# Kernel optimization log

Hardware: AMD Instinct MI355X
Metric: run time of the kernel (lower is better)

The kernel has to match this reference:

```python
import jax, jax.numpy as jnp
import numpy as np

B, T, H, L, V, S = 64, 256, 512, 64, 500, 3
TEMP_B = 1.0
EPS = 1e-17
NEG_INF = -1e9


def setup_inputs() -> dict:
    key = jax.random.key(0)
    ks = jax.random.split(key, 20)
    s = 0.02
    actions = jax.random.randint(ks[0], (B, T), 0, V)
    lengths = jax.random.randint(ks[1], (B,), 1, T + 1)
    u = jax.random.uniform(ks[2], (S - 1, B, T), minval=1e-6, maxval=1.0 - 1e-6)
    gumbel_b = -jnp.log(-jnp.log(u))                      # Gumbel(0,1) noise for boundary sampling
    eps_z = jax.random.normal(ks[3], (S, B, L))            # N(0,1) noise for gaussian latents
    embed = jax.random.normal(ks[4], (V, H)) * s
    Wx = jax.random.normal(ks[5], (H, 4 * H)) * s          # LSTM kernel (gate order i,f,g,o)
    Wh = jax.random.normal(ks[6], (H, 4 * H)) * s          # LSTM recurrent kernel
    b_lstm = jnp.zeros((4 * H,)).at[H:2 * H].set(1.0)      # unit forget bias (keras default)
    Wz1 = jax.random.normal(ks[7], (H, H)) * s
    bz1 = jnp.zeros((H,))
    Wz2 = jax.random.normal(ks[8], (H, 2 * L)) * s         # gaussian head -> [mu, log_var]
    bz2 = jnp.zeros((2 * L,))
    Wb1 = jax.random.normal(ks[9], (H, H)) * s
    bb1 = jnp.zeros((H,))
    Wb2 = jax.random.normal(ks[10], (H, 1)) * s
    bb2 = jnp.zeros((1,))
    Wd1 = jax.random.normal(ks[11], (L, H)) * s
    bd1 = jnp.zeros((H,))
    Wd2 = jax.random.normal(ks[12], (H, V)) * s
    bd2 = jnp.zeros((V,))
    return dict(actions=actions, lengths=lengths, gumbel_b=gumbel_b, eps_z=eps_z,
                embed=embed, Wx=Wx, Wh=Wh, b_lstm=b_lstm,
                Wz1=Wz1, bz1=bz1, Wz2=Wz2, bz2=bz2,
                Wb1=Wb1, bb1=bb1, Wb2=Wb2, bb2=bb2,
                Wd1=Wd1, bd1=bd1, Wd2=Wd2, bd2=bd2)


def _masked_encode(x, mask, Wx, Wh, b):
    """Masked LSTM: state is multiplied by mask[:, t] after every step."""
    def step(carry, inp):
        h, c = carry
        x_t, m_t = inp
        z = x_t @ Wx + h @ Wh + b
        i, f, g, o = jnp.split(z, 4, axis=-1)
        c_new = jax.nn.sigmoid(f) * c + jax.nn.sigmoid(i) * jnp.tanh(g)
        h_new = jax.nn.sigmoid(o) * jnp.tanh(c_new)
        m = m_t[:, None]
        return (m * h_new, m * c_new), h_new  # outputs are pre-mask h (as in source)
    h0 = jnp.zeros((x.shape[0], Wh.shape[0]), x.dtype)
    _, outs = jax.lax.scan(step, (h0, h0), (jnp.swapaxes(x, 0, 1), mask.T))
    return jnp.swapaxes(outs, 0, 1)  # [B,T,H]


def reference(actions, lengths, gumbel_b, eps_z, embed, Wx, Wh, b_lstm,
              Wz1, bz1, Wz2, bz2, Wb1, bb1, Wb2, bb2, Wd1, bd1, Wd2, bd2):
    emb = embed[actions]                       # [B,T,H]
    mask = jnp.ones((B, T), emb.dtype)
    encs, recs, masks = [], [], []
    logits_b_all, sample_b_all = [], []
    logits_z_all, sample_z_all = [], []
    for seg in range(S):
        enc = _masked_encode(emb, mask, Wx, Wh, b_lstm)
        encs.append(enc)
        if seg == S - 1:
            sample_b = jax.nn.one_hot(lengths - 1, T, dtype=emb.dtype)
        else:
            hid = jax.nn.relu(enc @ Wb1 + bb1)
            logits = (hid @ Wb2 + bb2)[..., 0]            # [B,T]
            logits = jnp.concatenate(
                [jnp.full((B, 1), NEG_INF, logits.dtype), logits[:, 1:]], axis=1)
            sample_b = jax.nn.softmax((logits + gumbel_b[seg]) / TEMP_B, axis=1)
            logits_b_all.append(logits)
        sample_b_all.append(sample_b)
        # latent readout (segment endpoint weighted sum)
        readout = jnp.sum(enc[:, :-1] * sample_b[:, 1:, None], axis=1)  # [B,H]
        hz = jax.nn.relu(readout @ Wz1 + bz1)
        logits_z = hz @ Wz2 + bz2                          # [B,2L]
        mu, log_var = jnp.split(logits_z, 2, axis=1)
        sample_z = mu + jnp.exp(0.5 * log_var) * eps_z[seg]
        logits_z_all.append(logits_z)
        sample_z_all.append(sample_z)
        # next-segment RNN mask: product of cumsums of all boundary samples so far
        if seg < S - 1:
            log_cums = [jnp.log(jnp.cumsum(bb, axis=1) + EPS) for bb in sample_b_all]
            mask = jnp.exp(sum(log_cums))
            masks.append(mask)
        # decode: single step from z, repeated over full sequence
        hd = jax.nn.relu(sample_z @ Wd1 + bd1)
        pred = hd @ Wd2 + bd2                              # [B,V]
        recs.append(jnp.broadcast_to(pred[:, None, :], (B, T, V)))
    return (jnp.stack(encs), jnp.stack(recs), jnp.stack(masks),
            jnp.stack(logits_b_all), jnp.stack(sample_b_all),
            jnp.stack(logits_z_all), jnp.stack(sample_z_all))
```

## Files before the change

### kernel.cpp

```cpp
#include <hip/hip_runtime.h>
#include <cstdint>
#include <cstddef>

typedef unsigned short ubf;
typedef unsigned int   u32;
typedef __attribute__((ext_vector_type(8))) short short8;
typedef __attribute__((ext_vector_type(4))) float f32x4;
typedef __attribute__((ext_vector_type(4))) float f4v;
typedef __attribute__((ext_vector_type(2))) float f2v;
typedef __attribute__((ext_vector_type(4))) unsigned short us4;

#define NEG_INF_F (-1000000000.0f)
#define FOURH 2048

#define ENC_SEG   8388608
#define REC_OFF   25165824
#define REC_SEG   8192000
#define MASK_OFF  49741824
#define LOGB_OFF  49774592
#define SAMB_OFF  49807360
#define LOGZ_OFF  49856512
#define SAMZ_OFF  49881088

#define SCR_P       0
#define SCR_HBUF    524288
#define SCR_FLAGS   557056
#define SCR_MASKF   558080
#define SCR_LOGCUM  574464
#define SCR_PART    590848
#define SCR_ENCB    1048576

__device__ __forceinline__ float bf2f(ubf u){
  union { u32 i; float f; } v; v.i = ((u32)u) << 16; return v.f;
}
__device__ __forceinline__ ubf f2bf(float f){
  union { float f; u32 i; } v; v.f = f;
  u32 x = v.i;
  u32 r = (x + 0x7FFFu + ((x >> 16) & 1u)) >> 16;
  return (ubf)r;
}
__device__ __forceinline__ float sigm(float x){
  return 1.0f / (1.0f + __expf(-x));
}
__device__ __forceinline__ float tanh_fast(float x){
  x = fminf(fmaxf(x, -20.0f), 20.0f);
  float e2 = __expf(2.0f * x);
  return (e2 - 1.0f) / (e2 + 1.0f);
}

__global__ void init_kernel(u32* flags){
  int tid = threadIdx.x;
  #pragma unroll
  for (int i = 0; i < 4; i++) flags[tid + i*256] = 0u;
}

__global__ __launch_bounds__(256, 2) void gemm_kernel(
    const void* __restrict__ Aptr, int a_f32,
    const float* __restrict__ Bf, const float* __restrict__ bias,
    ubf* __restrict__ C, const float* __restrict__ wb2, float* __restrict__ part,
    int M, int N, int K, int relu, int mclamp)
{
  __shared__ __align__(16) ubf As[128*40];
  __shared__ __align__(16) ubf Bs[128*40];
  int tid  = threadIdx.x;
  int bn   = blockIdx.x, bm = blockIdx.y;
  int w    = tid >> 6, lane = tid & 63, quad = lane >> 4, l16 = lane & 15;
  int wm   = w >> 1, wn = w & 1;

  f32x4 acc[4][4];
  #pragma unroll
  for (int i = 0; i < 4; i++)
    #pragma unroll
    for (int j = 0; j < 4; j++)
      #pragma unroll
      for (int r = 0; r < 4; r++) acc[i][j][r] = 0.0f;

  for (int k0 = 0; k0 < K; k0 += 32) {
    if (a_f32){
      const float* Af = (const float*)Aptr;
      #pragma unroll
      for (int h = 0; h < 4; h++){
        int v   = tid + h*256;
        int row = v >> 3, kc = (v & 7) * 4;
        int rm  = bm*128 + row;
        int ar  = rm < mclamp ? rm : mclamp;
        f4v q = *(const f4v*)(Af + (size_t)ar * K + k0 + kc);
        us4 s; s[0]=f2bf(q[0]); s[1]=f2bf(q[1]); s[2]=f2bf(q[2]); s[3]=f2bf(q[3]);
        *(us4*)&As[row*40 + kc] = s;
      }
    } else {
      const ubf* Ab = (const ubf*)Aptr;
      #pragma unroll
      for (int h = 0; h < 2; h++){
        int v   = tid + h*256;
        int row = v >> 2, kc = (v & 3) * 8;
        int rm  = bm*128 + row;
        int ar  = rm < mclamp ? rm : mclamp;
        uint4 q = *(const uint4*)(Ab + (size_t)ar * K + k0 + kc);
        *(uint4*)&As[row*40 + kc] = q;
      }
    }
    #pragma unroll
    for (int h = 0; h < 4; h++){
      int v  = tid + h*256;
      int kk = v >> 5, nn = (v & 31) * 4;
      f4v q = *(const f4v*)(Bf + (size_t)(k0 + kk) * N + bn*128 + nn);
      #pragma unroll
      for (int j = 0; j < 4; j++) Bs[(nn + j)*40 + kk] = f2bf(q[j]);
    }
    __syncthreads();
    short8 af[4], bfr[4];
    #pragma unroll
    for (int i = 0; i < 4; i++){
      int row = wm*64 + i*16 + l16;
      af[i]  = *(const short8*)&As[row*40 + quad*8];
      int col = wn*64 + i*16 + l16;
      bfr[i] = *(const short8*)&Bs[col*40 + quad*8];
    }
    #pragma unroll
    for (int i = 0; i < 4; i++)
      #pragma unroll
      for (int j = 0; j < 4; j++)
        acc[i][j] = __builtin_amdgcn_mfma_f32_16x16x32_bf16(af[i], bfr[j], acc[i][j], 0, 0, 0);
    __syncthreads();
  }
  if (!wb2){
    #pragma unroll
    for (int i = 0; i < 4; i++){
      #pragma unroll
      for (int j = 0; j < 4; j++){
        int n   = bn*128 + wn*64 + j*16 + l16;
        float bv = bias ? bias[n] : 0.0f;
        #pragma unroll
        for (int r = 0; r < 4; r++){
          int m   = bm*128 + wm*64 + i*16 + quad*4 + r;
          float vv = acc[i][j][r] + bv;
          if (relu) vv = fmaxf(vv, 0.0f);
          C[(size_t)m * N + n] = f2bf(vv);
        }
      }
    }
  } else {
    #pragma unroll
    for (int i = 0; i < 4; i++){
      f32x4 rp;
      #pragma unroll
      for (int r = 0; r < 4; r++) rp[r] = 0.0f;
      #pragma unroll
      for (int j = 0; j < 4; j++){
        int n   = bn*128 + wn*64 + j*16 + l16;
        float bv = bias[n];
        float wv = wb2[n];
        #pragma unroll
        for (int r = 0; r < 4; r++)
          rp[r] += fmaxf(acc[i][j][r] + bv, 0.0f) * wv;
      }
      #pragma unroll
      for (int off = 1; off < 16; off <<= 1)
        #pragma unroll
        for (int r = 0; r < 4; r++)
          rp[r] += __shfl_xor(rp[r], off, 64);
      if (l16 == 0){
        #pragma unroll
        for (int r = 0; r < 4; r++){
          int m = bm*128 + wm*64 + i*16 + quad*4 + r;
          part[(size_t)(bn*2 + wn)*16384 + m] = rp[r];
        }
      }
    }
  }
}

__device__ void tail_block(int b,
    const float* __restrict__ enc,
    const float* __restrict__ sb_g,
    const float* __restrict__ Wz1, const float* __restrict__ bz1,
    const float* __restrict__ Wz2, const float* __restrict__ bz2,
    const float* __restrict__ epsz,
    const float* __restrict__ Wd1, const float* __restrict__ bd1,
    const float* __restrict__ Wd2, const float* __restrict__ bd2,
    float* __restrict__ lzout, float* __restrict__ szout,
    float* __restrict__ recseg)
{
  __shared__ float sb[256];
  __shared__ float r[512];
  __shared__ float hz[512];
  __shared__ float lz[128];
  __shared__ float sz[64];
  __shared__ float hd[512];
  int tid = threadIdx.x;
  sb[tid] = sb_g[b*256 + tid];
  __syncthreads();
  {
    const float* base = enc + ((size_t)b*256)*512 + tid*2;
    float a0 = 0.0f, a1 = 0.0f;
    for (int t = 0; t < 255; t++){
      float m = sb[t + 1];
      f2v q = *(const f2v*)(base + (size_t)t*512);
      a0 += m * q[0];
      a1 += m * q[1];
    }
    r[tid*2]     = a0;
    r[tid*2 + 1] = a1;
  }
  __syncthreads();
  {
    float a0 = bz1[tid], a1 = bz1[tid + 256];
    for (int i = 0; i < 512; i++){
      float ri = r[i];
      a0 += ri * Wz1[(size_t)i*512 + tid];
      a1 += ri * Wz1[(size_t)i*512 + tid + 256];
    }
    hz[tid]       = fmaxf(a0, 0.0f);
    hz[tid + 256] = fmaxf(a1, 0.0f);
  }
  __syncthreads();
  if (tid < 128){
    float a = bz2[tid];
    for (int i = 0; i < 512; i++) a += hz[i] * Wz2[(size_t)i*128 + tid];
    lz[tid] = a;
    lzout[b*128 + tid] = a;
  }
  __syncthreads();
  if (tid < 64){
    float mu = lz[tid], lv = lz[64 + tid];
    float v = mu + __expf(0.5f * lv) * epsz[b*64 + tid];
    sz[tid] = v;
    szout[b*64 + tid] = v;
  }
  __syncthreads();
  {
    float a0 = bd1[tid], a1 = bd1[tid + 256];
    for (int l = 0; l < 64; l++){
      float s = sz[l];
      a0 += s * Wd1[l*512 + tid];
      a1 += s * Wd1[l*512 + tid + 256];
    }
    hd[tid]       = fmaxf(a0, 0.0f);
    hd[tid + 256] = fmaxf(a1, 0.0f);
  }
  __syncthreads();
  {
    float a0 = bd2[tid];
    float a1 = (tid < 244) ? bd2[tid + 256] : 0.0f;
    for (int h = 0; h < 512; h++){
      float hh = hd[h];
      a0 += hh * Wd2[(size_t)h*500 + tid];
      if (tid < 244) a1 += hh * Wd2[(size_t)h*500 + tid + 256];
    }
    for (int t = 0; t < 256; t++){
      float* row = recseg + (size_t)b*128000 + (size_t)t*500;
      row[tid] = a0;
      if (tid < 244) row[tid + 256] = a1;
    }
  }
}

__global__ __launch_bounds__(256, 1) void lstm_kernel(
    const ubf* __restrict__ Pt,
    const int* __restrict__ actions,
    const float* __restrict__ Whf,
    const float* __restrict__ mask,
    float* __restrict__ enc,
    ubf* __restrict__ encb,
    ubf* hbuf,
    u32* flags,
    int seg,
    const float* __restrict__ tenc, const float* __restrict__ tsb,
    const float* __restrict__ teps,
    const float* __restrict__ Wz1, const float* __restrict__ bz1,
    const float* __restrict__ Wz2, const float* __restrict__ bz2,
    const float* __restrict__ Wd1, const float* __restrict__ bd1,
    const float* __restrict__ Wd2, const float* __restrict__ bd2,
    float* __restrict__ tlz, float* __restrict__ tsz, float* __restrict__ trec)
{
  if (blockIdx.x >= 64){
    tail_block(blockIdx.x - 64, tenc, tsb, Wz1, bz1, Wz2, bz2, teps,
               Wd1, bd1, Wd2, bd2, tlz, tsz, trec);
    return;
  }
  __shared__ __align__(16) ubf   htile[16*520];
  __shared__ __align__(16) ubf   ptile[16*136];
  __shared__ __align__(16) float ztile[16*132];

  int tid  = threadIdx.x;
  int wv   = tid >> 6;
  int lane = tid & 63, quad = lane >> 4, l16 = lane & 15;
  int bg   = blockIdx.x >> 4, cg = blockIdx.x & 15;
  int j0   = cg * 32;

  short8 bfrag[2][16];
  #pragma unroll
  for (int h = 0; h < 2; h++){
    int col = wv*512 + j0 + h*16 + l16;
    #pragma unroll
    for (int kt = 0; kt < 16; kt++){
      short8 t8;
      #pragma unroll
      for (int j = 0; j < 8; j++){
        int k = kt*32 + quad*8 + j;
        t8[j] = (short)f2bf(Whf[(size_t)k * FOURH + col]);
      }
      bfrag[h][kt] = t8;
    }
  }

  float cst0 = 0.0f, cst1 = 0.0f;
  int bl = tid >> 4;
  int up = (tid & 15) * 2;
  int bglob = bg*16 + bl;
  u32* htile32 = (u32*)htile;
  unsigned epoch0 = (unsigned)seg * 256u;
  u32* myflag = &flags[(bg*16 + (tid >> 4))*16];

  for (int t = 0; t < 256; ++t){
    {
      int act  = actions[(size_t)bglob * 256 + t];
      int colc = (tid & 15) * 8;
      int gate = colc >> 5, cw = colc & 31;
      uint4 q = *(const uint4*)(Pt + (size_t)act * FOURH + gate*512 + j0 + cw);
      *(uint4*)&ptile[bl*136 + colc] = q;
    }
    if (t > 0){
      unsigned tgt = epoch0 + (unsigned)t;
      while (__hip_atomic_load(myflag, __ATOMIC_RELAXED, __HIP_MEMORY_SCOPE_AGENT) < tgt)
        __builtin_amdgcn_s_sleep(1);
      const u32* src = (const u32*)(hbuf + (size_t)(((t+1)&1)*4 + bg) * 16 * 512);
      u32 tmp[16];
      #pragma unroll
      for (int i = 0; i < 16; i++)
        tmp[i] = __hip_atomic_load(&src[tid + 256*i], __ATOMIC_RELAXED, __HIP_MEMORY_SCOPE_AGENT);
      #pragma unroll
      for (int i = 0; i < 16; i++)
        htile32[i*260 + tid] = tmp[i];
    }
    __syncthreads();

    f32x4 a0, a1;
    #pragma unroll
    for (int r = 0; r < 4; r++){ a0[r] = 0.0f; a1[r] = 0.0f; }
    if (t > 0){
      #pragma unroll
      for (int kt = 0; kt < 16; kt++){
        short8 af = *(const short8*)&htile[l16*520 + kt*32 + quad*8];
        a0 = __builtin_amdgcn_mfma_f32_16x16x32_bf16(af, bfrag[0][kt], a0, 0, 0, 0);
        a1 = __builtin_amdgcn_mfma_f32_16x16x32_bf16(af, bfrag[1][kt], a1, 0, 0, 0);
      }
    }
    #pragma unroll
    for (int r = 0; r < 4; r++){
      ztile[(quad*4 + r)*132 + wv*32 + l16]      = a0[r];
      ztile[(quad*4 + r)*132 + wv*32 + 16 + l16] = a1[r];
    }
    __syncthreads();

    float m = mask ? mask[(size_t)bglob * 256 + t] : 1.0f;
    f2v ev;
    ubf hp[2];
    #pragma unroll
    for (int p = 0; p < 2; p++){
      int u = up + p;
      float zi = ztile[bl*132 +       u] + bf2f(ptile[bl*136 +       u]);
      float zf = ztile[bl*132 + 32 + u] + bf2f(ptile[bl*136 + 32 + u]);
      float zg = ztile[bl*132 + 64 + u] + bf2f(ptile[bl*136 + 64 + u]);
      float zo = ztile[bl*132 + 96 + u] + bf2f(ptile[bl*136 + 96 + u]);
      float is = sigm(zi), fs = sigm(zf), gt = tanh_fast(zg), os = sigm(zo);
      float cp = p ? cst1 : cst0;
      float cn = fs * cp + is * gt;
      float hn = os * tanh_fast(cn);
      ev[p] = hn;
      float cm = m * cn;
      if (p) cst1 = cm; else cst0 = cm;
      hp[p] = f2bf(m * hn);
    }
    {
      u32 hword = (u32)hp[0] | ((u32)hp[1] << 16);
      u32* dst = (u32*)(hbuf + (size_t)((t&1)*4 + bg) * 16 * 512);
      __hip_atomic_store(&dst[(bl*512 + j0 + up) >> 1], hword,
                         __ATOMIC_RELAXED, __HIP_MEMORY_SCOPE_AGENT);
    }
    __threadfence_block();
    __syncthreads();
    if (tid == 0)
      __hip_atomic_store(&flags[(bg*16 + cg)*16], epoch0 + (unsigned)t + 1u,
                         __ATOMIC_RELAXED, __HIP_MEMORY_SCOPE_AGENT);
    *(f2v*)(enc + ((size_t)bglob * 256 + t) * 512 + j0 + up) = ev;
    if (encb){
      u32 ebw = (u32)f2bf(ev[0]) | ((u32)f2bf(ev[1]) << 16);
      *(u32*)&encb[((size_t)bglob * 256 + t) * 512 + j0 + up] = ebw;
    }
  }
}

__global__ __launch_bounds__(512, 1) void zdec2_kernel(
    const float* __restrict__ enc, const int* __restrict__ lengths,
    const float* __restrict__ Wz1, const float* __restrict__ bz1,
    const float* __restrict__ Wz2, const float* __restrict__ bz2,
    const float* __restrict__ epsz,
    const float* __restrict__ Wd1, const float* __restrict__ bd1,
    const float* __restrict__ Wd2, const float* __restrict__ bd2,
    float* __restrict__ lzout, float* __restrict__ szout, float* __restrict__ recseg)
{
  __shared__ float r[512], hz[512], lz[128], sz[64], hd[512];
  __shared__ __align__(16) float row[500];
  int b = blockIdx.x, tid = threadIdx.x;
  int L = lengths[b];
  r[tid] = (L >= 2) ? enc[((size_t)b*256 + (L - 2))*512 + tid] : 0.0f;
  __syncthreads();
  {
    float a0 = bz1[tid];
    for (int i = 0; i < 512; i++)
      a0 += r[i] * Wz1[(size_t)i*512 + tid];
    hz[tid] = fmaxf(a0, 0.0f);
  }
  __syncthreads();
  if (tid < 128){
    float a = bz2[tid];
    for (int i = 0; i < 512; i++) a += hz[i] * Wz2[(size_t)i*128 + tid];
    lz[tid] = a;
    lzout[b*128 + tid] = a;
  }
  __syncthreads();
  if (tid < 64){
    float mu = lz[tid], lv = lz[64 + tid];
    float v = mu + __expf(0.5f * lv) * epsz[b*64 + tid];
    sz[tid] = v;
    szout[b*64 + tid] = v;
  }
  __syncthreads();
  {
    float a0 = bd1[tid];
    for (int l = 0; l < 64; l++)
      a0 += sz[l] * Wd1[l*512 + tid];
    hd[tid] = fmaxf(a0, 0.0f);
  }
  __syncthreads();
  if (tid < 500){
    float a0 = bd2[tid];
    for (int h = 0; h < 512; h++)
      a0 += hd[h] * Wd2[(size_t)h*500 + tid];
    row[tid] = a0;
  }
  __syncthreads();
  for (int i = tid; i < 256*125; i += 512){
    int t = i / 125, c = i - t*125;
    *(f4v*)(recseg + (size_t)b*128000 + (size_t)t*500 + c*4) = *(const f4v*)&row[c*4];
  }
}

__global__ __launch_bounds__(256, 4) void softmax_kernel(
    const float* __restrict__ part, const float* __restrict__ bb2, const float* __restrict__ gum,
    float* __restrict__ lout,
    float* __restrict__ sbout,
    float* __restrict__ logcum, float* __restrict__ maskf, float* __restrict__ maskout,
    int seg)
{
  __shared__ float red[256];
  __shared__ float cs[256];
  int b = blockIdx.x, t = threadIdx.x;
  float raw = 0.0f;
  #pragma unroll
  for (int s = 0; s < 8; s++) raw += part[s*16384 + b*256 + t];
  float lg  = (t == 0) ? NEG_INF_F : (raw + bb2[0]);
  lout[b*256 + t] = lg;
  float x = lg + gum[b*256 + t];
  red[t] = x; __syncthreads();
  for (int o = 128; o > 0; o >>= 1){ if (t < o) red[t] = fmaxf(red[t], red[t+o]); __syncthreads(); }
  float mx = red[0]; __syncthreads();
  float e = __expf(x - mx);
  red[t] = e; __syncthreads();
  for (int o = 128; o > 0; o >>= 1){ if (t < o) red[t] += red[t+o]; __syncthreads(); }
  float s = red[0];
  float sb = e / s;
  sbout[b*256 + t] = sb;
  cs[t] = sb; __syncthreads();
  for (int o = 1; o < 256; o <<= 1){
    float v = cs[t];
    if (t >= o) v += cs[t - o];
    __syncthreads();
    cs[t] = v;
    __syncthreads();
  }
  float lc = logf(cs[t] + 1e-17f);
  float acc = (seg == 0) ? lc : (logcum[b*256 + t] + lc);
  logcum[b*256 + t] = acc;
  float mk = __expf(acc);
  maskf[b*256 + t] = mk;
  maskout[b*256 + t] = mk;
}

__global__ void onehot_kernel(const int* __restrict__ lengths,
                              float* __restrict__ sbout)
{
  int b = blockIdx.x, t = threadIdx.x;
  sbout[b*256 + t] = (t == (lengths[b] - 1)) ? 1.0f : 0.0f;
}

extern "C" void kernel_launch(void* const* d_in, const int* in_sizes, int n_in,
                              void* d_out, int out_size, void* d_ws, size_t ws_size,
                              hipStream_t stream)
{
  const int*   actions = (const int*)d_in[0];
  const int*   lengths = (const int*)d_in[1];
  const float* gumbel  = (const float*)d_in[2];
  const float* epsz    = (const float*)d_in[3];
  const float* embed   = (const float*)d_in[4];
  const float* Wx      = (const float*)d_in[5];
  const float* Wh      = (const float*)d_in[6];
  const float* b_lstm  = (const float*)d_in[7];
  const float* Wz1     = (const float*)d_in[8];
  const float* bz1     = (const float*)d_in[9];
  const float* Wz2     = (const float*)d_in[10];
  const float* bz2     = (const float*)d_in[11];
  const float* Wb1     = (const float*)d_in[12];
  const float* bb1     = (const float*)d_in[13];
  const float* Wb2     = (const float*)d_in[14];
  const float* bb2     = (const float*)d_in[15];
  const float* Wd1     = (const float*)d_in[16];
  const float* bd1     = (const float*)d_in[17];
  const float* Wd2     = (const float*)d_in[18];
  const float* bd2     = (const float*)d_in[19];
  float* out = (float*)d_out;

  float* r2      = out + (size_t)REC_OFF + 2*(size_t)REC_SEG;
  ubf*   P       = (ubf*)(r2 + SCR_P);
  ubf*   hbuf    = (ubf*)(r2 + SCR_HBUF);
  u32*   flags   = (u32*)(r2 + SCR_FLAGS);
  float* maskf   = r2 + SCR_MASKF;
  float* logcum  = r2 + SCR_LOGCUM;
  float* partf   = r2 + SCR_PART;
  ubf*   encb    = (ubf*)(r2 + SCR_ENCB);

  hipLaunchKernelGGL(init_kernel, dim3(1), dim3(256), 0, stream, flags);

  hipLaunchKernelGGL(gemm_kernel, dim3(16, 4), dim3(256), 0, stream,
                     (const void*)embed, 1, Wx, b_lstm, P,
                     (const float*)nullptr, (float*)nullptr,
                     512, 2048, 512, 0, 499);

  for (int seg = 0; seg < 3; ++seg){
    int prev = (seg > 0) ? (seg - 1) : 0;
    hipLaunchKernelGGL(lstm_kernel, dim3((seg == 0) ? 64 : 128), dim3(256), 0, stream,
                       P, actions, Wh,
                       (seg == 0) ? (const float*)nullptr : maskf,
                       out + (size_t)seg * ENC_SEG,
                       (seg < 2) ? encb : (ubf*)nullptr,
                       hbuf, flags, seg,
                       out + (size_t)prev * ENC_SEG,
                       out + SAMB_OFF + (size_t)prev * 16384,
                       epsz + (size_t)prev * 4096,
                       Wz1, bz1, Wz2, bz2, Wd1, bd1, Wd2, bd2,
                       out + LOGZ_OFF + (size_t)prev * 8192,
                       out + SAMZ_OFF + (size_t)prev * 4096,
                       out + REC_OFF + (size_t)prev * REC_SEG);
    if (seg < 2){
      hipLaunchKernelGGL(gemm_kernel, dim3(4, 128), dim3(256), 0, stream,
                         (const void*)encb, 0, Wb1, bb1, (ubf*)nullptr, Wb2, partf,
                         16384, 512, 512, 1, 16383);
      hipLaunchKernelGGL(softmax_kernel, dim3(64), dim3(256), 0, stream,
                         partf, bb2, gumbel + (size_t)seg * 16384,
                         out + LOGB_OFF + (size_t)seg * 16384,
                         out + SAMB_OFF + (size_t)seg * 16384,
                         logcum, maskf, out + MASK_OFF + (size_t)seg * 16384, seg);
    } else {
      hipLaunchKernelGGL(onehot_kernel, dim3(64), dim3(256), 0, stream,
                         lengths, out + SAMB_OFF + (size_t)seg * 16384);
      hipLaunchKernelGGL(zdec2_kernel, dim3(64), dim3(512), 0, stream,
                         out + (size_t)seg * ENC_SEG, lengths,
                         Wz1, bz1, Wz2, bz2,
                         epsz + (size_t)seg * 4096,
                         Wd1, bd1, Wd2, bd2,
                         out + LOGZ_OFF + (size_t)seg * 8192,
                         out + SAMZ_OFF + (size_t)seg * 4096,
                         out + REC_OFF + (size_t)seg * REC_SEG);
    }
  }
  (void)in_sizes; (void)n_in; (void)out_size; (void)d_ws; (void)ws_size;
}
```

Measured before the change: 2.203 ms.

## Fuse LSTM, boundary GEMM and softmax into one persistent kernel per segment

Merges the per-segment LSTM recurrence, the boundary-head GEMM and the Gumbel softmax/mask kernel into a single launch. GEMM blocks spin on per-timestep LSTM flags so they can start on early timesteps while the recurrence is still running, and softmax blocks wait on a completion counter. The bf16 encoder copy is stored time-major so that each GEMM row tile corresponds to a prefix of timesteps. The one-hot kernel is folded into zdec2. This is meant to hide the boundary GEMM behind the serial LSTM and remove launch gaps. The risk is deadlock or contention if the spinning blocks are not co-resident with the LSTM blocks, plus extra atomic-store overhead.

```diff
diff --git a/kernel.cpp b/kernel.cpp
--- a/kernel.cpp
+++ b/kernel.cpp
@@ -28,6 +28,8 @@
 #define SCR_MASKF   558080
 #define SCR_LOGCUM  574464
 #define SCR_PART    590848
+#define SCR_SENT    721920
+#define SCR_CNT     722944
 #define SCR_ENCB    1048576
 
 __device__ __forceinline__ float bf2f(ubf u){
@@ -48,10 +50,11 @@
   return (e2 - 1.0f) / (e2 + 1.0f);
 }
 
-__global__ void init_kernel(u32* flags){
+__global__ void init_kernel(u32* flags, u32* sent, u32* cnt){
   int tid = threadIdx.x;
   #pragma unroll
-  for (int i = 0; i < 4; i++) flags[tid + i*256] = 0u;
+  for (int i = 0; i < 4; i++){ flags[tid + i*256] = 0u; sent[tid + i*256] = 0u; }
+  if (tid < 32) cnt[tid] = 0u;
 }
 
 __global__ __launch_bounds__(256, 2) void gemm_kernel(
@@ -124,23 +127,197 @@
         acc[i][j] = __builtin_amdgcn_mfma_f32_16x16x32_bf16(af[i], bfr[j], acc[i][j], 0, 0, 0);
     __syncthreads();
   }
-  if (!wb2){
-    #pragma unroll
-    for (int i = 0; i < 4; i++){
-      #pragma unroll
-      for (int j = 0; j < 4; j++){
-        int n   = bn*128 + wn*64 + j*16 + l16;
-        float bv = bias ? bias[n] : 0.0f;
+  #pragma unroll
+  for (int i = 0; i < 4; i++){
+    #pragma unroll
+    for (int j = 0; j < 4; j++){
+      int n   = bn*128 + wn*64 + j*16 + l16;
+      float bv = bias ? bias[n] : 0.0f;
+      #pragma unroll
+      for (int r = 0; r < 4; r++){
+        int m   = bm*128 + wm*64 + i*16 + quad*4 + r;
+        float vv = acc[i][j][r] + bv;
+        if (relu) vv = fmaxf(vv, 0.0f);
+        C[(size_t)m * N + n] = f2bf(vv);
+      }
+    }
+  }
+  (void)wb2; (void)part; (void)M;
+}
+
+__device__ void tail_block(char* smem, int b,
+    const float* __restrict__ enc, const float* __restrict__ sb_g,
+    const float* __restrict__ Wz1, const float* __restrict__ bz1,
+    const float* __restrict__ Wz2, const float* __restrict__ bz2,
+    const float* __restrict__ epsz,
+    const float* __restrict__ Wd1, const float* __restrict__ bd1,
+    const float* __restrict__ Wd2, const float* __restrict__ bd2,
+    float* __restrict__ lzout, float* __restrict__ szout,
+    float* __restrict__ recseg)
+{
+  float* sb = (float*)smem;
+  float* r  = sb + 256;
+  float* hz = r + 512;
+  float* lz = hz + 512;
+  float* sz = lz + 128;
+  float* hd = sz + 64;
+  int tid = threadIdx.x;
+  sb[tid] = sb_g[b*256 + tid];
+  __syncthreads();
+  {
+    const float* base = enc + ((size_t)b*256)*512 + tid*2;
+    float a0 = 0.0f, a1 = 0.0f;
+    for (int t = 0; t < 255; t++){
+      float m = sb[t + 1];
+      f2v q = *(const f2v*)(base + (size_t)t*512);
+      a0 += m * q[0];
+      a1 += m * q[1];
+    }
+    r[tid*2]     = a0;
+    r[tid*2 + 1] = a1;
+  }
+  __syncthreads();
+  {
+    float a0 = bz1[tid], a1 = bz1[tid + 256];
+    for (int i = 0; i < 512; i++){
+      float ri = r[i];
+      a0 += ri * Wz1[(size_t)i*512 + tid];
+      a1 += ri * Wz1[(size_t)i*512 + tid + 256];
+    }
+    hz[tid]       = fmaxf(a0, 0.0f);
+    hz[tid + 256] = fmaxf(a1, 0.0f);
+  }
+  __syncthreads();
+  if (tid < 128){
+    float a = bz2[tid];
+    for (int i = 0; i < 512; i++) a += hz[i] * Wz2[(size_t)i*128 + tid];
+    lz[tid] = a;
+    lzout[b*128 + tid] = a;
+  }
+  __syncthreads();
+  if (tid < 64){
+    float mu = lz[tid], lv = lz[64 + tid];
+    float v = mu + __expf(0.5f * lv) * epsz[b*64 + tid];
+    sz[tid] = v;
+    szout[b*64 + tid] = v;
+  }
+  __syncthreads();
+  {
+    float a0 = bd1[tid], a1 = bd1[tid + 256];
+    for (int l = 0; l < 64; l++){
+      float s = sz[l];
+      a0 += s * Wd1[l*512 + tid];
+      a1 += s * Wd1[l*512 + tid + 256];
+    }
+    hd[tid]       = fmaxf(a0, 0.0f);
+    hd[tid + 256] = fmaxf(a1, 0.0f);
+  }
+  __syncthreads();
+  {
+    float a0 = bd2[tid];
+    float a1 = (tid < 244) ? bd2[tid + 256] : 0.0f;
+    for (int h = 0; h < 512; h++){
+      float hh = hd[h];
+      a0 += hh * Wd2[(size_t)h*500 + tid];
+      if (tid < 244) a1 += hh * Wd2[(size_t)h*500 + tid + 256];
+    }
+    for (int t = 0; t < 256; t++){
+      float* row = recseg + (size_t)b*128000 + (size_t)t*500;
+      row[tid] = a0;
+      if (tid < 244) row[tid + 256] = a1;
+    }
+  }
+}
+
+__global__ __launch_bounds__(256, 1) void mega_kernel(
+    int seg,
+    const ubf* __restrict__ Pt, const int* __restrict__ actions,
+    const float* __restrict__ Whf, const float* __restrict__ mask,
+    float* __restrict__ enc, ubf* __restrict__ encb,
+    ubf* hbuf, u32* flags, u32* sent,
+    const float* __restrict__ Wb1, const float* __restrict__ bb1,
+    const float* __restrict__ Wb2f, float* __restrict__ part, u32* gemmcnt,
+    const float* __restrict__ bb2, const float* __restrict__ gum,
+    float* __restrict__ lout, float* __restrict__ sbout,
+    float* __restrict__ logcum, float* __restrict__ maskf, float* __restrict__ maskoutp,
+    const float* __restrict__ tenc, const float* __restrict__ tsb,
+    const float* __restrict__ teps,
+    const float* __restrict__ Wz1, const float* __restrict__ bz1,
+    const float* __restrict__ Wz2, const float* __restrict__ bz2,
+    const float* __restrict__ Wd1, const float* __restrict__ bd1,
+    const float* __restrict__ Wd2, const float* __restrict__ bd2,
+    float* __restrict__ tlz, float* __restrict__ tsz, float* __restrict__ trec)
+{
+  __shared__ __align__(16) char smem[29696];
+  int bx  = threadIdx.y ? 0 : blockIdx.x;
+  int tid = threadIdx.x;
+  unsigned epoch0 = (unsigned)seg * 256u;
+  int gemm_base = (seg == 0) ? 64 : 128;
+
+  if (seg >= 1 && bx >= 64 && bx < 128){
+    tail_block(smem, bx - 64, tenc, tsb, Wz1, bz1, Wz2, bz2, teps,
+               Wd1, bd1, Wd2, bd2, tlz, tsz, trec);
+    return;
+  }
+
+  if (seg < 2 && bx >= gemm_base && bx < gemm_base + 512){
+    int gb = bx - gemm_base;
+    int bn = gb & 3, bm = gb >> 2;
+    {
+      int need = bm*2 + 3;
+      unsigned tgt = epoch0 + (unsigned)(need > 256 ? 256 : need);
+      if (tid < 64){
+        while (__hip_atomic_load(&flags[tid*16], __ATOMIC_RELAXED, __HIP_MEMORY_SCOPE_AGENT) < tgt)
+          __builtin_amdgcn_s_sleep(16);
+        if (bm == 127){
+          while (__hip_atomic_load(&sent[tid*16], __ATOMIC_RELAXED, __HIP_MEMORY_SCOPE_AGENT) < (u32)(seg + 1))
+            __builtin_amdgcn_s_sleep(16);
+        }
+      }
+      __syncthreads();
+    }
+    ubf* As = (ubf*)smem;
+    ubf* Bs = (ubf*)smem + 128*40;
+    int w = tid >> 6, lane = tid & 63, quad = lane >> 4, l16 = lane & 15;
+    int wm = w >> 1, wn = w & 1;
+    f32x4 acc[4][4];
+    #pragma unroll
+    for (int i = 0; i < 4; i++)
+      #pragma unroll
+      for (int j = 0; j < 4; j++)
         #pragma unroll
-        for (int r = 0; r < 4; r++){
-          int m   = bm*128 + wm*64 + i*16 + quad*4 + r;
-          float vv = acc[i][j][r] + bv;
-          if (relu) vv = fmaxf(vv, 0.0f);
-          C[(size_t)m * N + n] = f2bf(vv);
-        }
-      }
-    }
-  } else {
+        for (int r = 0; r < 4; r++) acc[i][j][r] = 0.0f;
+    for (int k0 = 0; k0 < 512; k0 += 32){
+      #pragma unroll
+      for (int h = 0; h < 2; h++){
+        int v   = tid + h*256;
+        int row = v >> 2, kc = (v & 3) * 8;
+        int m   = bm*128 + row;
+        uint4 q = *(const uint4*)(encb + (size_t)m * 512 + k0 + kc);
+        *(uint4*)&As[row*40 + kc] = q;
+      }
+      #pragma unroll
+      for (int h = 0; h < 4; h++){
+        int v  = tid + h*256;
+        int kk = v >> 5, nn = (v & 31) * 4;
+        f4v q = *(const f4v*)(Wb1 + (size_t)(k0 + kk) * 512 + bn*128 + nn);
+        #pragma unroll
+        for (int j = 0; j < 4; j++) Bs[(nn + j)*40 + kk] = f2bf(q[j]);
+      }
+      __syncthreads();
+      short8 af[4], bfr[4];
+      #pragma unroll
+      for (int i = 0; i < 4; i++){
+        af[i]  = *(const short8*)&As[(wm*64 + i*16 + l16)*40 + quad*8];
+        bfr[i] = *(const short8*)&Bs[(wn*64 + i*16 + l16)*40 + quad*8];
+      }
+      #pragma unroll
+      for (int i = 0; i < 4; i++)
+        #pragma unroll
+        for (int j = 0; j < 4; j++)
+          acc[i][j] = __builtin_amdgcn_mfma_f32_16x16x32_bf16(af[i], bfr[j], acc[i][j], 0, 0, 0);
+      __syncthreads();
+    }
     #pragma unroll
     for (int i = 0; i < 4; i++){
       f32x4 rp;
@@ -148,9 +325,9 @@
       for (int r = 0; r < 4; r++) rp[r] = 0.0f;
       #pragma unroll
       for (int j = 0; j < 4; j++){
-        int n   = bn*128 + wn*64 + j*16 + l16;
-        float bv = bias[n];
-        float wv = wb2[n];
+        int n = bn*128 + wn*64 + j*16 + l16;
+        float bv = bb1[n];
+        float wv = Wb2f[n];
         #pragma unroll
         for (int r = 0; r < 4; r++)
           rp[r] += fmaxf(acc[i][j][r] + bv, 0.0f) * wv;
@@ -164,129 +341,66 @@
         #pragma unroll
         for (int r = 0; r < 4; r++){
           int m = bm*128 + wm*64 + i*16 + quad*4 + r;
-          part[(size_t)(bn*2 + wn)*16384 + m] = rp[r];
+          __hip_atomic_store(&part[(size_t)(bn*2 + wn)*16384 + m], rp[r],
+                             __ATOMIC_RELAXED, __HIP_MEMORY_SCOPE_AGENT);
         }
       }
     }
-  }
-}
-
-__device__ void tail_block(int b,
-    const float* __restrict__ enc,
-    const float* __restrict__ sb_g,
-    const float* __restrict__ Wz1, const float* __restrict__ bz1,
-    const float* __restrict__ Wz2, const float* __restrict__ bz2,
-    const float* __restrict__ epsz,
-    const float* __restrict__ Wd1, const float* __restrict__ bd1,
-    const float* __restrict__ Wd2, const float* __restrict__ bd2,
-    float* __restrict__ lzout, float* __restrict__ szout,
-    float* __restrict__ recseg)
-{
-  __shared__ float sb[256];
-  __shared__ float r[512];
-  __shared__ float hz[512];
-  __shared__ float lz[128];
-  __shared__ float sz[64];
-  __shared__ float hd[512];
-  int tid = threadIdx.x;
-  sb[tid] = sb_g[b*256 + tid];
-  __syncthreads();
-  {
-    const float* base = enc + ((size_t)b*256)*512 + tid*2;
-    float a0 = 0.0f, a1 = 0.0f;
-    for (int t = 0; t < 255; t++){
-      float m = sb[t + 1];
-      f2v q = *(const f2v*)(base + (size_t)t*512);
-      a0 += m * q[0];
-      a1 += m * q[1];
-    }
-    r[tid*2]     = a0;
-    r[tid*2 + 1] = a1;
-  }
-  __syncthreads();
-  {
-    float a0 = bz1[tid], a1 = bz1[tid + 256];
-    for (int i = 0; i < 512; i++){
-      float ri = r[i];
-      a0 += ri * Wz1[(size_t)i*512 + tid];
-      a1 += ri * Wz1[(size_t)i*512 + tid + 256];
-    }
-    hz[tid]       = fmaxf(a0, 0.0f);
-    hz[tid + 256] = fmaxf(a1, 0.0f);
-  }
-  __syncthreads();
-  if (tid < 128){
-    float a = bz2[tid];
-    for (int i = 0; i < 512; i++) a += hz[i] * Wz2[(size_t)i*128 + tid];
-    lz[tid] = a;
-    lzout[b*128 + tid] = a;
-  }
-  __syncthreads();
-  if (tid < 64){
-    float mu = lz[tid], lv = lz[64 + tid];
-    float v = mu + __expf(0.5f * lv) * epsz[b*64 + tid];
-    sz[tid] = v;
-    szout[b*64 + tid] = v;
-  }
-  __syncthreads();
-  {
-    float a0 = bd1[tid], a1 = bd1[tid + 256];
-    for (int l = 0; l < 64; l++){
-      float s = sz[l];
-      a0 += s * Wd1[l*512 + tid];
-      a1 += s * Wd1[l*512 + tid + 256];
-    }
-    hd[tid]       = fmaxf(a0, 0.0f);
-    hd[tid + 256] = fmaxf(a1, 0.0f);
-  }
-  __syncthreads();
-  {
-    float a0 = bd2[tid];
-    float a1 = (tid < 244) ? bd2[tid + 256] : 0.0f;
-    for (int h = 0; h < 512; h++){
-      float hh = hd[h];
-      a0 += hh * Wd2[(size_t)h*500 + tid];
-      if (tid < 244) a1 += hh * Wd2[(size_t)h*500 + tid + 256];
-    }
-    for (int t = 0; t < 256; t++){
-      float* row = recseg + (size_t)b*128000 + (size_t)t*500;
-      row[tid] = a0;
-      if (tid < 244) row[tid + 256] = a1;
-    }
-  }
-}
-
-__global__ __launch_bounds__(256, 1) void lstm_kernel(
-    const ubf* __restrict__ Pt,
-    const int* __restrict__ actions,
-    const float* __restrict__ Whf,
-    const float* __restrict__ mask,
-    float* __restrict__ enc,
-    ubf* __restrict__ encb,
-    ubf* hbuf,
-    u32* flags,
-    int seg,
-    const float* __restrict__ tenc, const float* __restrict__ tsb,
-    const float* __restrict__ teps,
-    const float* __restrict__ Wz1, const float* __restrict__ bz1,
-    const float* __restrict__ Wz2, const float* __restrict__ bz2,
-    const float* __restrict__ Wd1, const float* __restrict__ bd1,
-    const float* __restrict__ Wd2, const float* __restrict__ bd2,
-    float* __restrict__ tlz, float* __restrict__ tsz, float* __restrict__ trec)
-{
-  if (blockIdx.x >= 64){
-    tail_block(blockIdx.x - 64, tenc, tsb, Wz1, bz1, Wz2, bz2, teps,
-               Wd1, bd1, Wd2, bd2, tlz, tsz, trec);
+    asm volatile("s_waitcnt vmcnt(0)" ::: "memory");
+    __syncthreads();
+    if (tid == 0) atomicAdd(&gemmcnt[seg], 1u);
     return;
   }
-  __shared__ __align__(16) ubf   htile[16*520];
-  __shared__ __align__(16) ubf   ptile[16*136];
-  __shared__ __align__(16) float ztile[16*132];
-
-  int tid  = threadIdx.x;
+
+  if (seg < 2 && bx >= gemm_base + 512){
+    int b = bx - (gemm_base + 512);
+    if (tid == 0){
+      while (__hip_atomic_load(&gemmcnt[seg], __ATOMIC_RELAXED, __HIP_MEMORY_SCOPE_AGENT) < 512u)
+        __builtin_amdgcn_s_sleep(16);
+    }
+    __syncthreads();
+    float* red = (float*)smem;
+    float* cs  = red + 256;
+    int t = tid;
+    float raw = 0.0f;
+    #pragma unroll
+    for (int s = 0; s < 8; s++) raw += part[s*16384 + t*64 + b];
+    float lg = (t == 0) ? NEG_INF_F : (raw + bb2[0]);
+    lout[b*256 + t] = lg;
+    float x = lg + gum[b*256 + t];
+    red[t] = x; __syncthreads();
+    for (int o = 128; o > 0; o >>= 1){ if (t < o) red[t] = fmaxf(red[t], red[t+o]); __syncthreads(); }
+    float mx = red[0]; __syncthreads();
+    float e = __expf(x - mx);
+    red[t] = e; __syncthreads();
+    for (int o = 128; o > 0; o >>= 1){ if (t < o) red[t] += red[t+o]; __syncthreads(); }
+    float s = red[0];
+    float sb = e / s;
+    sbout[b*256 + t] = sb;
+    cs[t] = sb; __syncthreads();
+    for (int o = 1; o < 256; o <<= 1){
+      float v = cs[t];
+      if (t >= o) v += cs[t - o];
+      __syncthreads();
+      cs[t] = v;
+      __syncthreads();
+    }
+    float lc = logf(cs[t] + 1e-17f);
+    float acc2 = (seg == 0) ? lc : (logcum[b*256 + t] + lc);
+    logcum[b*256 + t] = acc2;
+    float mk = __expf(acc2);
+    maskf[b*256 + t] = mk;
+    maskoutp[b*256 + t] = mk;
+    return;
+  }
+
+  ubf*   htile = (ubf*)smem;
+  ubf*   ptile = (ubf*)(smem + 16640);
+  float* ztile = (float*)(smem + 20992);
+
   int wv   = tid >> 6;
   int lane = tid & 63, quad = lane >> 4, l16 = lane & 15;
-  int bg   = blockIdx.x >> 4, cg = blockIdx.x & 15;
+  int bg   = bx >> 4, cg = bx & 15;
   int j0   = cg * 32;
 
   short8 bfrag[2][16];
@@ -310,7 +424,6 @@
   int up = (tid & 15) * 2;
   int bglob = bg*16 + bl;
   u32* htile32 = (u32*)htile;
-  unsigned epoch0 = (unsigned)seg * 256u;
   u32* myflag = &flags[(bg*16 + (tid >> 4))*16];
 
   for (int t = 0; t < 256; ++t){
@@ -387,9 +500,14 @@
     *(f2v*)(enc + ((size_t)bglob * 256 + t) * 512 + j0 + up) = ev;
     if (encb){
       u32 ebw = (u32)f2bf(ev[0]) | ((u32)f2bf(ev[1]) << 16);
-      *(u32*)&encb[((size_t)bglob * 256 + t) * 512 + j0 + up] = ebw;
-    }
-  }
+      __hip_atomic_store((u32*)(encb + ((size_t)t*64 + bglob)*512 + j0 + up), ebw,
+                         __ATOMIC_RELAXED, __HIP_MEMORY_SCOPE_AGENT);
+    }
+  }
+  asm volatile("s_waitcnt vmcnt(0)" ::: "memory");
+  if (tid == 0)
+    __hip_atomic_store(&sent[(bg*16 + cg)*16], (u32)(seg + 1),
+                       __ATOMIC_RELAXED, __HIP_MEMORY_SCOPE_AGENT);
 }
 
 __global__ __launch_bounds__(512, 1) void zdec2_kernel(
@@ -399,12 +517,14 @@
     const float* __restrict__ epsz,
     const float* __restrict__ Wd1, const float* __restrict__ bd1,
     const float* __restrict__ Wd2, const float* __restrict__ bd2,
-    float* __restrict__ lzout, float* __restrict__ szout, float* __restrict__ recseg)
+    float* __restrict__ lzout, float* __restrict__ szout, float* __restrict__ recseg,
+    float* __restrict__ sbout2)
 {
   __shared__ float r[512], hz[512], lz[128], sz[64], hd[512];
   __shared__ __align__(16) float row[500];
   int b = blockIdx.x, tid = threadIdx.x;
   int L = lengths[b];
+  if (tid < 256) sbout2[b*256 + tid] = (tid == (L - 1)) ? 1.0f : 0.0f;
   r[tid] = (L >= 2) ? enc[((size_t)b*256 + (L - 2))*512 + tid] : 0.0f;
   __syncthreads();
   {
@@ -446,54 +566,6 @@
     int t = i / 125, c = i - t*125;
     *(f4v*)(recseg + (size_t)b*128000 + (size_t)t*500 + c*4) = *(const f4v*)&row[c*4];
   }
-}
-
-__global__ __launch_bounds__(256, 4) void softmax_kernel(
-    const float* __restrict__ part, const float* __restrict__ bb2, const float* __restrict__ gum,
-    float* __restrict__ lout,
-    float* __restrict__ sbout,
-    float* __restrict__ logcum, float* __restrict__ maskf, float* __restrict__ maskout,
-    int seg)
-{
-  __shared__ float red[256];
-  __shared__ float cs[256];
-  int b = blockIdx.x, t = threadIdx.x;
-  float raw = 0.0f;
-  #pragma unroll
-  for (int s = 0; s < 8; s++) raw += part[s*16384 + b*256 + t];
-  float lg  = (t == 0) ? NEG_INF_F : (raw + bb2[0]);
-  lout[b*256 + t] = lg;
-  float x = lg + gum[b*256 + t];
-  red[t] = x; __syncthreads();
-  for (int o = 128; o > 0; o >>= 1){ if (t < o) red[t] = fmaxf(red[t], red[t+o]); __syncthreads(); }
-  float mx = red[0]; __syncthreads();
-  float e = __expf(x - mx);
-  red[t] = e; __syncthreads();
-  for (int o = 128; o > 0; o >>= 1){ if (t < o) red[t] += red[t+o]; __syncthreads(); }
-  float s = red[0];
-  float sb = e / s;
-  sbout[b*256 + t] = sb;
-  cs[t] = sb; __syncthreads();
-  for (int o = 1; o < 256; o <<= 1){
-    float v = cs[t];
-    if (t >= o) v += cs[t - o];
-    __syncthreads();
-    cs[t] = v;
-    __syncthreads();
-  }
-  float lc = logf(cs[t] + 1e-17f);
-  float acc = (seg == 0) ? lc : (logcum[b*256 + t] + lc);
-  logcum[b*256 + t] = acc;
-  float mk = __expf(acc);
-  maskf[b*256 + t] = mk;
-  maskout[b*256 + t] = mk;
-}
-
-__global__ void onehot_kernel(const int* __restrict__ lengths,
-                              float* __restrict__ sbout)
-{
-  int b = blockIdx.x, t = threadIdx.x;
-  sbout[b*256 + t] = (t == (lengths[b] - 1)) ? 1.0f : 0.0f;
 }
 
 extern "C" void kernel_launch(void* const* d_in, const int* in_sizes, int n_in,
@@ -529,9 +601,11 @@
   float* maskf   = r2 + SCR_MASKF;
   float* logcum  = r2 + SCR_LOGCUM;
   float* partf   = r2 + SCR_PART;
+  u32*   sent    = (u32*)(r2 + SCR_SENT);
+  u32*   cnt     = (u32*)(r2 + SCR_CNT);
   ubf*   encb    = (ubf*)(r2 + SCR_ENCB);
 
-  hipLaunchKernelGGL(init_kernel, dim3(1), dim3(256), 0, stream, flags);
+  hipLaunchKernelGGL(init_kernel, dim3(1), dim3(256), 0, stream, flags, sent, cnt);
 
   hipLaunchKernelGGL(gemm_kernel, dim3(16, 4), dim3(256), 0, stream,
                      (const void*)embed, 1, Wx, b_lstm, P,
@@ -540,12 +614,19 @@
 
   for (int seg = 0; seg < 3; ++seg){
     int prev = (seg > 0) ? (seg - 1) : 0;
-    hipLaunchKernelGGL(lstm_kernel, dim3((seg == 0) ? 64 : 128), dim3(256), 0, stream,
+    int grid = (seg == 0) ? 640 : (seg == 1) ? 704 : 128;
+    hipLaunchKernelGGL(mega_kernel, dim3(grid), dim3(256), 0, stream,
+                       seg,
                        P, actions, Wh,
                        (seg == 0) ? (const float*)nullptr : maskf,
                        out + (size_t)seg * ENC_SEG,
                        (seg < 2) ? encb : (ubf*)nullptr,
-                       hbuf, flags, seg,
+                       hbuf, flags, sent,
+                       Wb1, bb1, Wb2, partf, cnt,
+                       bb2, gumbel + (size_t)seg * 16384,
+                       out + LOGB_OFF + (size_t)seg * 16384,
+                       out + SAMB_OFF + (size_t)seg * 16384,
+                       logcum, maskf, out + MASK_OFF + (size_t)seg * 16384,
                        out + (size_t)prev * ENC_SEG,
                        out + SAMB_OFF + (size_t)prev * 16384,
                        epsz + (size_t)prev * 4096,
@@ -553,27 +634,15 @@
                        out + LOGZ_OFF + (size_t)prev * 8192,
                        out + SAMZ_OFF + (size_t)prev * 4096,
                        out + REC_OFF + (size_t)prev * REC_SEG);
-    if (seg < 2){
-      hipLaunchKernelGGL(gemm_kernel, dim3(4, 128), dim3(256), 0, stream,
-                         (const void*)encb, 0, Wb1, bb1, (ubf*)nullptr, Wb2, partf,
-                         16384, 512, 512, 1, 16383);
-      hipLaunchKernelGGL(softmax_kernel, dim3(64), dim3(256), 0, stream,
-                         partf, bb2, gumbel + (size_t)seg * 16384,
-                         out + LOGB_OFF + (size_t)seg * 16384,
-                         out + SAMB_OFF + (size_t)seg * 16384,
-                         logcum, maskf, out + MASK_OFF + (size_t)seg * 16384, seg);
-    } else {
-      hipLaunchKernelGGL(onehot_kernel, dim3(64), dim3(256), 0, stream,
-                         lengths, out + SAMB_OFF + (size_t)seg * 16384);
-      hipLaunchKernelGGL(zdec2_kernel, dim3(64), dim3(512), 0, stream,
-                         out + (size_t)seg * ENC_SEG, lengths,
-                         Wz1, bz1, Wz2, bz2,
-                         epsz + (size_t)seg * 4096,
-                         Wd1, bd1, Wd2, bd2,
-                         out + LOGZ_OFF + (size_t)seg * 8192,
-                         out + SAMZ_OFF + (size_t)seg * 4096,
-                         out + REC_OFF + (size_t)seg * REC_SEG);
-    }
-  }
+  }
+  hipLaunchKernelGGL(zdec2_kernel, dim3(64), dim3(512), 0, stream,
+                     out + (size_t)2 * ENC_SEG, lengths,
+                     Wz1, bz1, Wz2, bz2,
+                     epsz + (size_t)2 * 4096,
+                     Wd1, bd1, Wd2, bd2,
+                     out + LOGZ_OFF + (size_t)2 * 8192,
+                     out + SAMZ_OFF + (size_t)2 * 4096,
+                     out + REC_OFF + (size_t)2 * REC_SEG,
+                     out + SAMB_OFF + (size_t)2 * 16384);
   (void)in_sizes; (void)n_in; (void)out_size; (void)d_ws; (void)ws_size;
 }
```

After: 2.176 ms. No clear change (-1.2%).
